# Performance work log

Measured on AMD Instinct MI355X. Metric: run time of the kernel, lower is better.

## Reference

```python
import jax, jax.numpy as jnp
import numpy as np

N = 100000      # nodes
E = 1600000     # edges (avg degree 16)
F_IN = 32       # node_features
F_OUT = 32      # filters
K = 2           # Chebyshev order


def setup_inputs() -> dict:
    key = jax.random.key(0)
    ks = jax.random.split(key, 8)
    x = jax.random.normal(ks[0], (N, F_IN), dtype=jnp.float32)
    edge_index = jax.random.randint(ks[1], (2, E), 0, N, dtype=jnp.int32).astype(jnp.int64)
    edge_weight = jax.random.uniform(ks[2], (E,), dtype=jnp.float32)
    s_in = 1.0 / np.sqrt(F_IN)
    s_out = 1.0 / np.sqrt(F_OUT)
    # gate order: i, f, c, o
    Wx = jax.random.normal(ks[3], (4, K, F_IN, F_OUT), dtype=jnp.float32) * s_in
    bx = jnp.zeros((4, F_OUT), dtype=jnp.float32)
    Wh = jax.random.normal(ks[4], (4, K, F_OUT, F_OUT), dtype=jnp.float32) * s_out
    bh = jnp.zeros((4, F_OUT), dtype=jnp.float32)
    wc = jax.random.normal(ks[5], (3, F_OUT), dtype=jnp.float32) * 0.1  # peephole i, f, o
    b_gate = jnp.zeros((4, F_OUT), dtype=jnp.float32)
    lin_w = jax.random.normal(ks[6], (F_OUT, 1), dtype=jnp.float32) * s_out
    lin_b = jnp.zeros((1,), dtype=jnp.float32)
    return dict(x=x, edge_index=edge_index, edge_weight=edge_weight, Wx=Wx, bx=bx,
                Wh=Wh, bh=bh, wc=wc, b_gate=b_gate, lin_w=lin_w, lin_b=lin_b)


def _cheb_norm(src, dst, w, num_nodes):
    # ChebConv 'sym' normalization with lambda_max = 2.0:
    # scaled Laplacian L_hat = L_sym - I has zero diagonal; off-diagonal entries are
    # -D^{-1/2} A D^{-1/2}. Self loops removed (equivalently: weight zeroed).
    w = jnp.where(src == dst, 0.0, w)
    deg = jax.ops.segment_sum(w, src, num_segments=num_nodes)
    dinv = jnp.where(deg > 0, jax.lax.rsqrt(jnp.where(deg > 0, deg, 1.0)), 0.0)
    return -dinv[src] * w * dinv[dst]


def _forward(x, src, dst, norm, Wx, bx, Wh, bh, wc, b_gate, lin_w, lin_b):
    n = x.shape[0]

    def cheb(inp, W, b):
        # K=2 Chebyshev conv: Tx_0 = inp, Tx_1 = L_hat @ inp (sparse gather/scatter)
        tx1 = jax.ops.segment_sum(norm[:, None] * inp[src], dst, num_segments=n)
        return inp @ W[0] + tx1 @ W[1] + b

    H = jnp.zeros((n, Wh.shape[-1]), dtype=x.dtype)
    C = jnp.zeros_like(H)
    I = jax.nn.sigmoid(cheb(x, Wx[0], bx[0]) + cheb(H, Wh[0], bh[0]) + wc[0] * C + b_gate[0])
    Fg = jax.nn.sigmoid(cheb(x, Wx[1], bx[1]) + cheb(H, Wh[1], bh[1]) + wc[1] * C + b_gate[1])
    T = jnp.tanh(cheb(x, Wx[2], bx[2]) + cheb(H, Wh[2], bh[2]) + b_gate[2])
    C = Fg * C + I * T
    O = jax.nn.sigmoid(cheb(x, Wx[3], bx[3]) + cheb(H, Wh[3], bh[3]) + wc[2] * C + b_gate[3])
    H = O * jnp.tanh(C)
    return jax.nn.relu(H) @ lin_w + lin_b  # [N, 1]


def reference(x, edge_index, edge_weight, Wx, bx, Wh, bh, wc, b_gate, lin_w, lin_b):
    src, dst = edge_index[0], edge_index[1]
    norm = _cheb_norm(src, dst, edge_weight, x.shape[0])
    return _forward(x, src, dst, norm, Wx, bx, Wh, bh, wc, b_gate, lin_w, lin_b)
```

## Files before the change

kernel.cpp:

```cpp
#include <hip/hip_runtime.h>


#define FDIM 32
#define MAX_N 100000
#define MAX_E 1600000
#define CBSH 8
#define CB 256
#define MAX_NB ((MAX_N + CB - 1) / CB)
#define NBLK 512
#define SCAN_TILE 2048
#define GNB 64
#define PERBLK 3136

typedef int   iv4 __attribute__((ext_vector_type(4)));
typedef float fv4 __attribute__((ext_vector_type(4)));
__device__ __forceinline__ iv4 nt_i4(const int* p)   { return __builtin_nontemporal_load((const iv4*)p); }
__device__ __forceinline__ fv4 nt_f4(const float* p) { return __builtin_nontemporal_load((const fv4*)p); }

__device__ float g_deg[MAX_N];
__device__ int   g_part2[2 * MAX_NB * NBLK + 1];
__device__ int   g_blk[1024];
__device__ uint2 g_rec[MAX_E];
__device__ uint2 g_srec[MAX_E];
__device__ int   g_row[MAX_N + 1];
__device__ __attribute__((aligned(16))) int   g_src2[MAX_E];
__device__ __attribute__((aligned(16))) float g_nrm2[MAX_E];
__device__ __attribute__((aligned(16))) float g_xs2[MAX_N * FDIM];
__device__ float g_tx1[MAX_N * FDIM];

__global__ __launch_bounds__(256) void hist2_kernel(const int* __restrict__ ei,
                                                    int E, int n_nodes, int nbuck,
                                                    int per_blk) {
    __shared__ int hd[MAX_NB];
    __shared__ int hs[MAX_NB];
    for (int i = threadIdx.x; i < nbuck; i += 256) { hd[i] = 0; hs[i] = 0; }
    __syncthreads();
    int start = blockIdx.x * per_blk;
    int end = start + per_blk;
    if (end > E) end = E;
    for (int base = start; base < end; base += 1024) {
        int e = base + threadIdx.x * 4;
        if (e + 4 <= end) {
            int4 s4 = *(const int4*)(ei + e);
            int4 d4 = *(const int4*)(ei + E + e);
#define H2(S, D) if ((unsigned)(S) < (unsigned)n_nodes && (unsigned)(D) < (unsigned)n_nodes) { \
                atomicAdd(&hd[(D) >> CBSH], 1); atomicAdd(&hs[(S) >> CBSH], 1); }
            H2(s4.x, d4.x) H2(s4.y, d4.y) H2(s4.z, d4.z) H2(s4.w, d4.w)
#undef H2
        } else if (e < end) {
            for (int q = e; q < end; ++q) {
                int s = ei[q], d = ei[E + q];
                if ((unsigned)s >= (unsigned)n_nodes || (unsigned)d >= (unsigned)n_nodes)
                    continue;
                atomicAdd(&hd[d >> CBSH], 1);
                atomicAdd(&hs[s >> CBSH], 1);
            }
        }
    }
    __syncthreads();
    for (int i = threadIdx.x; i < nbuck; i += 256) {
        g_part2[i * NBLK + blockIdx.x] = hd[i];
        g_part2[(nbuck + i) * NBLK + blockIdx.x] = hs[i];
    }
    if (blockIdx.x == 0 && threadIdx.x == 0)
        g_part2[2 * nbuck * NBLK] = 0;
}

__global__ __launch_bounds__(256) void scan1_kernel(int n) {
    __shared__ int sh[256];
    int tid = threadIdx.x;
    int base = blockIdx.x * SCAN_TILE + tid * 8;
    int v[8];
#pragma unroll
    for (int i = 0; i < 8; ++i) v[i] = (base + i < n) ? g_part2[base + i] : 0;
    int tsum = 0;
#pragma unroll
    for (int i = 0; i < 8; ++i) tsum += v[i];
    sh[tid] = tsum;
    __syncthreads();
    for (int off = 1; off < 256; off <<= 1) {
        int t = (tid >= off) ? sh[tid - off] : 0;
        __syncthreads();
        sh[tid] += t;
        __syncthreads();
    }
    if (tid == 255) g_blk[blockIdx.x] = sh[255];
    int run = sh[tid] - tsum;
#pragma unroll
    for (int i = 0; i < 8; ++i) {
        if (base + i < n) g_part2[base + i] = run;
        run += v[i];
    }
}

__global__ __launch_bounds__(256) void scatter_burst_kernel(const int* __restrict__ ei,
                                                            const float* __restrict__ w,
                                                            int E, int n_nodes, int nbuck,
                                                            int per_blk, int ntile) {
    __shared__ int   toff[256];
    __shared__ int   cnt[512];
    __shared__ int   sc[512];
    __shared__ int   gb[MAX_NB];
    __shared__ int   cur[MAX_NB];
    __shared__ uint2 staged[PERBLK];
    __shared__ int   gpos[PERBLK];
    int tid = threadIdx.x;
    int blk = blockIdx.x;
    int start = blk * per_blk;
    int end = start + per_blk;
    if (end > E) end = E;

    int orig = (tid < ntile) ? g_blk[tid] : 0;
    toff[tid] = orig;
    __syncthreads();
    for (int off = 1; off < 256; off <<= 1) {
        int v = (tid >= off) ? toff[tid - off] : 0;
        __syncthreads();
        toff[tid] += v;
        __syncthreads();
    }
    toff[tid] -= orig;
    __syncthreads();
#define SCN(idx) (g_part2[idx] + toff[(idx) >> 11])

    for (int phase = 0; phase < 2; ++phase) {
        cnt[tid] = 0; cnt[tid + 256] = 0;
        __syncthreads();
        for (int i = tid; i < nbuck; i += 256) {
            int flat = (phase * nbuck + i) * NBLK + blk;
            int g0 = SCN(flat);
            int g1 = SCN(flat + 1);
            gb[i] = g0 - phase * E;
            cnt[i] = g1 - g0;
        }
        __syncthreads();
        sc[tid] = cnt[tid]; sc[tid + 256] = cnt[tid + 256];
        __syncthreads();
        for (int off = 1; off < 512; off <<= 1) {
            int v0 = (tid >= off) ? sc[tid - off] : 0;
            int v1 = sc[tid + 256 - off];
            __syncthreads();
            sc[tid] += v0; sc[tid + 256] += v1;
            __syncthreads();
        }
        for (int i = tid; i < nbuck; i += 256) cur[i] = sc[i] - cnt[i];
        __syncthreads();
#define SB1(S, D, W)                                                            \
        {   int s = (S), d = (D);                                               \
            if ((unsigned)s < (unsigned)n_nodes && (unsigned)d < (unsigned)n_nodes) { \
                int key = phase ? s : d;                                        \
                int bin = key >> CBSH;                                          \
                float w0 = (s == d) ? 0.f : (W);           \
                unsigned pay = phase ? (unsigned)(s & (CB - 1))                 \
                    : (((unsigned)s << CBSH) | (unsigned)(d & (CB - 1)));       \
                int p = atomicAdd(&cur[bin], 1);                \
                staged[p] = make_uint2(pay, __float_as_uint(w0));               \
                gpos[p] = gb[bin] + (p - (sc[bin] - cnt[bin]));                 \
            } }
        for (int base = start; base < end; base += 1024) {
            int e = base + tid * 4;
            if (e + 4 <= end) {
                iv4 s4 = nt_i4(ei + e);
                iv4 d4 = nt_i4(ei + E + e);
                fv4 w4 = nt_f4(w + e);
                SB1(s4[0], d4[0], w4[0]) SB1(s4[1], d4[1], w4[1])
                SB1(s4[2], d4[2], w4[2]) SB1(s4[3], d4[3], w4[3])
            } else if (e < end) {
                for (int q = e; q < end; ++q) SB1(ei[q], ei[E + q], w[q])
            }
        }
#undef SB1
        __syncthreads();
        int tot = sc[511];
        if (phase == 0) {
            for (int t = tid; t < tot; t += 256) g_rec[gpos[t]] = staged[t];
        } else {
            for (int t = tid; t < tot; t += 256) g_srec[gpos[t]] = staged[t];
        }
        __syncthreads();
    }
#undef SCN
}

__global__ __launch_bounds__(1024) void sortdeg_kernel(const float* __restrict__ x,
                                                       int E, int n_nodes, int nbuck,
                                                       int ntile) {
    __shared__ int   toff[256];
    __shared__ int   cnt[CB];
    __shared__ int   cur[CB];
    __shared__ float ldeg[CB];
    __shared__ int   wsum[4];
    int tid = threadIdx.x;
    int b = blockIdx.x;

    int orig = 0;
    if (tid < 256) { orig = (tid < ntile) ? g_blk[tid] : 0; toff[tid] = orig; }
    __syncthreads();
    for (int off = 1; off < 256; off <<= 1) {
        int v = (tid < 256 && tid >= off) ? toff[tid - off] : 0;
        __syncthreads();
        if (tid < 256) toff[tid] += v;
        __syncthreads();
    }
    if (tid < 256) toff[tid] -= orig;
    if (tid < CB) { cnt[tid] = 0; ldeg[tid] = 0.f; }
    __syncthreads();
#define SCN(idx) (g_part2[idx] + toff[(idx) >> 11])
    int rsD = SCN(b * NBLK);
    int reD = SCN((b + 1) * NBLK);
    int rsS = SCN((nbuck + b) * NBLK) - E;
    int reS = SCN((nbuck + b + 1) * NBLK) - E;
#undef SCN

    for (int i = rsD + tid; i < reD; i += 1024)
        atomicAdd(&cnt[g_rec[i].x & (CB - 1)], 1);
    for (int i = rsS + tid; i < reS; i += 1024) {
        uint2 r = g_srec[i];
        atomicAdd(&ldeg[r.x], __uint_as_float(r.y));
    }
    __syncthreads();

    if (tid < CB) {
        float dg = ldeg[tid];
        float dv = (dg > 0.f) ? rsqrtf(dg) : 0.f;
        ldeg[tid] = dv;
        int node = (b << CBSH) + tid;
        if (node < n_nodes) g_deg[node] = dv;
    }
    __syncthreads();
    for (int t = tid; t < CB * FDIM / 4; t += 1024) {
        int q = t * 4;
        int loc = q >> 5;
        int node = (b << CBSH) + loc;
        if (node < n_nodes) {
            fv4 xv = *(const fv4*)&x[node * FDIM + (q & 31)];
            float dv = ldeg[loc];
            xv[0] *= dv; xv[1] *= dv; xv[2] *= dv; xv[3] *= dv;
            *(fv4*)&g_xs2[node * FDIM + (q & 31)] = xv;
        }
    }

    {
        int lane = tid & 63;
        int wave = tid >> 6;
        int v = (tid < CB) ? cnt[tid] : 0;
        int inc = v;
#pragma unroll
        for (int off = 1; off < 64; off <<= 1) {
            int t = __shfl_up(inc, off, 64);
            if (lane >= off) inc += t;
        }
        if (tid < CB && lane == 63) wsum[wave] = inc;
        __syncthreads();
        if (tid < CB) {
            int wo = 0;
#pragma unroll
            for (int ww = 0; ww < 4; ++ww) wo += (ww < wave) ? wsum[ww] : 0;
            int start = rsD + wo + (inc - v);
            cur[tid] = start;
            int node = (b << CBSH) + tid;
            if (node < n_nodes) g_row[node] = start;
        }
    }
    if (b == nbuck - 1 && tid == 0) g_row[n_nodes] = reD;
    __syncthreads();
    for (int i = rsD + tid; i < reD; i += 1024) {
        uint2 r = g_rec[i];
        int loc = r.x & (CB - 1);
        int pos = atomicAdd(&cur[loc], 1);
        g_src2[pos] = (int)(r.x >> CBSH);
        g_nrm2[pos] = -__uint_as_float(r.y);
    }
}

__global__ __launch_bounds__(256) void gather_kernel(int n_nodes) {
    int t = blockIdx.x * blockDim.x + threadIdx.x;
    int node = t >> 5;
    int f = t & 31;
    if (node >= n_nodes) return;
    int i = g_row[node];
    int end = g_row[node + 1];
    float acc = 0.f, accB = 0.f;
    while (i < end && (i & 3)) {
        acc += g_nrm2[i] * g_xs2[g_src2[i] * FDIM + f];
        ++i;
    }
    for (; i + 8 <= end; i += 8) {
        iv4 sa = nt_i4(g_src2 + i);
        iv4 sb = nt_i4(g_src2 + i + 4);
        fv4 na = nt_f4(g_nrm2 + i);
        fv4 nb = nt_f4(g_nrm2 + i + 4);
        float xa0 = g_xs2[sa[0] * FDIM + f], xa1 = g_xs2[sa[1] * FDIM + f];
        float xa2 = g_xs2[sa[2] * FDIM + f], xa3 = g_xs2[sa[3] * FDIM + f];
        float xb0 = g_xs2[sb[0] * FDIM + f], xb1 = g_xs2[sb[1] * FDIM + f];
        float xb2 = g_xs2[sb[2] * FDIM + f], xb3 = g_xs2[sb[3] * FDIM + f];
        acc  += na[0] * xa0 + na[1] * xa1 + na[2] * xa2 + na[3] * xa3;
        accB += nb[0] * xb0 + nb[1] * xb1 + nb[2] * xb2 + nb[3] * xb3;
    }
    for (; i + 4 <= end; i += 4) {
        iv4 s4 = nt_i4(g_src2 + i);
        fv4 n4 = nt_f4(g_nrm2 + i);
        acc += n4[0] * g_xs2[s4[0] * FDIM + f] + n4[1] * g_xs2[s4[1] * FDIM + f]
             + n4[2] * g_xs2[s4[2] * FDIM + f] + n4[3] * g_xs2[s4[3] * FDIM + f];
    }
    for (; i < end; ++i) acc += g_nrm2[i] * g_xs2[g_src2[i] * FDIM + f];
    float dvn = g_deg[node];
    g_tx1[node * FDIM + f] = dvn * (acc + accB);
}

__global__ __launch_bounds__(256, 4) void gates64_kernel(
    const float* __restrict__ x,
    const float* __restrict__ Wx, const float* __restrict__ bx,
    const float* __restrict__ bh, const float* __restrict__ wc,
    const float* __restrict__ bg, const float* __restrict__ lin_w,
    const float* __restrict__ lin_b, float* __restrict__ out, int n_nodes) {
    __shared__ float Ws[3 * 2048];
    __shared__ float xs[GNB * FDIM];
    __shared__ float ts[GNB * FDIM];

    for (int idx = threadIdx.x; idx < 512; idx += 256) {
        *(float4*)&Ws[idx * 4]        = *(const float4*)&Wx[0 * 2048 + idx * 4];
        *(float4*)&Ws[2048 + idx * 4] = *(const float4*)&Wx[2 * 2048 + idx * 4];
        *(float4*)&Ws[4096 + idx * 4] = *(const float4*)&Wx[3 * 2048 + idx * 4];
    }
    int node0 = blockIdx.x * GNB;
    for (int t = threadIdx.x; t < GNB * FDIM / 4; t += 256) {
        int q = t * 4;
        int n = node0 + (q >> 5);
        float4 xv = make_float4(0.f, 0.f, 0.f, 0.f);
        float4 tv = make_float4(0.f, 0.f, 0.f, 0.f);
        if (n < n_nodes) {
            xv = *(const float4*)&x[n * FDIM + (q & 31)];
            tv = *(const float4*)&g_tx1[n * FDIM + (q & 31)];
        }
        *(float4*)&xs[q] = xv;
        *(float4*)&ts[q] = tv;
    }
    __syncthreads();

    int j   = threadIdx.x & 31;
    int grp = threadIdx.x >> 5;

    float ai0=0.f,ai1=0.f,ai2=0.f,ai3=0.f,ai4=0.f,ai5=0.f,ai6=0.f,ai7=0.f;
    float ac0=0.f,ac1=0.f,ac2=0.f,ac3=0.f,ac4=0.f,ac5=0.f,ac6=0.f,ac7=0.f;
    float ao0=0.f,ao1=0.f,ao2=0.f,ao3=0.f,ao4=0.f,ao5=0.f,ao6=0.f,ao7=0.f;
    const float* xr = &xs[(grp * 8) * FDIM];
    const float* tr = &ts[(grp * 8) * FDIM];
    for (int k4 = 0; k4 < 32; k4 += 4) {
        float4 xv0 = *(const float4*)(xr + 0 * FDIM + k4);
        float4 xv1 = *(const float4*)(xr + 1 * FDIM + k4);
        float4 xv2 = *(const float4*)(xr + 2 * FDIM + k4);
        float4 xv3 = *(const float4*)(xr + 3 * FDIM + k4);
        float4 xv4 = *(const float4*)(xr + 4 * FDIM + k4);
        float4 xv5 = *(const float4*)(xr + 5 * FDIM + k4);
        float4 xv6 = *(const float4*)(xr + 6 * FDIM + k4);
        float4 xv7 = *(const float4*)(xr + 7 * FDIM + k4);
        float4 tv0 = *(const float4*)(tr + 0 * FDIM + k4);
        float4 tv1 = *(const float4*)(tr + 1 * FDIM + k4);
        float4 tv2 = *(const float4*)(tr + 2 * FDIM + k4);
        float4 tv3 = *(const float4*)(tr + 3 * FDIM + k4);
        float4 tv4 = *(const float4*)(tr + 4 * FDIM + k4);
        float4 tv5 = *(const float4*)(tr + 5 * FDIM + k4);
        float4 tv6 = *(const float4*)(tr + 6 * FDIM + k4);
        float4 tv7 = *(const float4*)(tr + 7 * FDIM + k4);
#define KSTEP(kc, COMP)                                        \
        {   int o0 = (k4 + kc) * 32 + j;                       \
            float wi0 = Ws[o0],        wi1 = Ws[1024 + o0];    \
            float wg0 = Ws[2048 + o0], wg1 = Ws[3072 + o0];    \
            float wo0 = Ws[4096 + o0], wo1 = Ws[5120 + o0];    \
            ai0 += xv0.COMP * wi0 + tv0.COMP * wi1;            \
            ac0 += xv0.COMP * wg0 + tv0.COMP * wg1;            \
            ao0 += xv0.COMP * wo0 + tv0.COMP * wo1;            \
            ai1 += xv1.COMP * wi0 + tv1.COMP * wi1;            \
            ac1 += xv1.COMP * wg0 + tv1.COMP * wg1;            \
            ao1 += xv1.COMP * wo0 + tv1.COMP * wo1;            \
            ai2 += xv2.COMP * wi0 + tv2.COMP * wi1;            \
            ac2 += xv2.COMP * wg0 + tv2.COMP * wg1;            \
            ao2 += xv2.COMP * wo0 + tv2.COMP * wo1;            \
            ai3 += xv3.COMP * wi0 + tv3.COMP * wi1;            \
            ac3 += xv3.COMP * wg0 + tv3.COMP * wg1;            \
            ao3 += xv3.COMP * wo0 + tv3.COMP * wo1;            \
            ai4 += xv4.COMP * wi0 + tv4.COMP * wi1;            \
            ac4 += xv4.COMP * wg0 + tv4.COMP * wg1;            \
            ao4 += xv4.COMP * wo0 + tv4.COMP * wo1;            \
            ai5 += xv5.COMP * wi0 + tv5.COMP * wi1;            \
            ac5 += xv5.COMP * wg0 + tv5.COMP * wg1;            \
            ao5 += xv5.COMP * wo0 + tv5.COMP * wo1;            \
            ai6 += xv6.COMP * wi0 + tv6.COMP * wi1;            \
            ac6 += xv6.COMP * wg0 + tv6.COMP * wg1;            \
            ao6 += xv6.COMP * wo0 + tv6.COMP * wo1;            \
            ai7 += xv7.COMP * wi0 + tv7.COMP * wi1;            \
            ac7 += xv7.COMP * wg0 + tv7.COMP * wg1;            \
            ao7 += xv7.COMP * wo0 + tv7.COMP * wo1;            \
        }
        KSTEP(0, x) KSTEP(1, y) KSTEP(2, z) KSTEP(3, w)
#undef KSTEP
    }

    float bi = bx[0 * 32 + j] + bh[0 * 32 + j] + bg[0 * 32 + j];
    float bc = bx[2 * 32 + j] + bh[2 * 32 + j] + bg[2 * 32 + j];
    float bo = bx[3 * 32 + j] + bh[3 * 32 + j] + bg[3 * 32 + j];
    float wcp = wc[2 * 32 + j];
    float lwj = lin_w[j];
    float lb0 = lin_b[0];

#define GOUT(m, AI, AC, AO)                                            \
    {   int n = node0 + grp * 8 + m;                                   \
        float I = 1.f / (1.f + __expf(-(AI + bi)));                    \
        float T = tanhf(AC + bc);                                      \
        float C = I * T;                                               \
        float O = 1.f / (1.f + __expf(-(AO + bo + wcp * C)));          \
        float H = O * tanhf(C);                                        \
        float r = fmaxf(H, 0.f) * lwj;                                 \
        _Pragma("unroll")                                              \
        for (int mm = 16; mm > 0; mm >>= 1) r += __shfl_xor(r, mm, 32);\
        if (j == 0 && n < n_nodes) out[n] = r + lb0; }
    GOUT(0, ai0, ac0, ao0) GOUT(1, ai1, ac1, ao1)
    GOUT(2, ai2, ac2, ao2) GOUT(3, ai3, ac3, ao3)
    GOUT(4, ai4, ac4, ao4) GOUT(5, ai5, ac5, ao5)
    GOUT(6, ai6, ac6, ao6) GOUT(7, ai7, ac7, ao7)
#undef GOUT
}

extern "C" void kernel_launch(void* const* d_in, const int* in_sizes, int n_in,
                              void* d_out, int out_size, void* d_ws, size_t ws_size,
                              hipStream_t stream) {
    const float* x     = (const float*)d_in[0];
    const int*   ei    = (const int*)d_in[1];
    const float* w     = (const float*)d_in[2];
    const float* Wx    = (const float*)d_in[3];
    const float* bx    = (const float*)d_in[4];
    const float* bh    = (const float*)d_in[6];
    const float* wc    = (const float*)d_in[7];
    const float* bg    = (const float*)d_in[8];
    const float* lin_w = (const float*)d_in[9];
    const float* lin_b = (const float*)d_in[10];
    float*       out   = (float*)d_out;

    int n_nodes = in_sizes[0] / FDIM;
    if (n_nodes > MAX_N) n_nodes = MAX_N;
    int E = in_sizes[2];
    if (E > MAX_E) E = MAX_E;

    int nbuck   = (n_nodes + CB - 1) >> CBSH;
    int per_blk = (((E + NBLK - 1) / NBLK) + 3) & ~3;
    int n_scan  = 2 * nbuck * NBLK + 1;
    int nb_scan = (n_scan + SCAN_TILE - 1) / SCAN_TILE;

    hist2_kernel<<<NBLK, 256, 0, stream>>>(ei, E, n_nodes, nbuck, per_blk);
    scan1_kernel<<<nb_scan, 256, 0, stream>>>(n_scan);
    scatter_burst_kernel<<<NBLK, 256, 0, stream>>>(ei, w, E, n_nodes, nbuck,
                                                   per_blk, nb_scan);
    sortdeg_kernel<<<nbuck, 1024, 0, stream>>>(x, E, n_nodes, nbuck, nb_scan);
    {
        long long tot = (long long)n_nodes * 32;
        gather_kernel<<<(int)((tot + 255) / 256), 256, 0, stream>>>(n_nodes);
    }
    gates64_kernel<<<(n_nodes + GNB - 1) / GNB, 256, 0, stream>>>(
        x, Wx, bx, bh, wc, bg, lin_w, lin_b, out, n_nodes);
}
```

Baseline: 254.7 us.

## Fold full symmetric normalization into edge weights and gather raw x

Splits the sort/degree kernel into a degree-sum kernel and a fine-sort kernel, so that all degrees exist before edges are placed. Each edge then stores its complete norm (-dinv[src]*w*dinv[dst]). This removes the pre-scaled copy of x (a full N×32 write plus read) and the per-node scale in the gather, which now reads x directly. In exchange it adds a kernel launch, a second pass over the scan offsets, and one random g_deg read per edge during the sort.

```diff
diff --git a/kernel.cpp b/kernel.cpp
--- a/kernel.cpp
+++ b/kernel.cpp
@@ -25,7 +25,6 @@
 __device__ int   g_row[MAX_N + 1];
 __device__ __attribute__((aligned(16))) int   g_src2[MAX_E];
 __device__ __attribute__((aligned(16))) float g_nrm2[MAX_E];
-__device__ __attribute__((aligned(16))) float g_xs2[MAX_N * FDIM];
 __device__ float g_tx1[MAX_N * FDIM];
 
 __global__ __launch_bounds__(256) void hist2_kernel(const int* __restrict__ ei,
@@ -182,17 +181,51 @@
 #undef SCN
 }
 
-__global__ __launch_bounds__(1024) void sortdeg_kernel(const float* __restrict__ x,
-                                                       int E, int n_nodes, int nbuck,
+__global__ __launch_bounds__(1024) void deg_sum_kernel(int E, int n_nodes, int nbuck,
                                                        int ntile) {
+    __shared__ int   toff[256];
+    __shared__ float ldeg[CB];
+    int tid = threadIdx.x;
+    int b = blockIdx.x;
+    int orig = 0;
+    if (tid < 256) { orig = (tid < ntile) ? g_blk[tid] : 0; toff[tid] = orig; }
+    __syncthreads();
+    for (int off = 1; off < 256; off <<= 1) {
+        int v = (tid < 256 && tid >= off) ? toff[tid - off] : 0;
+        __syncthreads();
+        if (tid < 256) toff[tid] += v;
+        __syncthreads();
+    }
+    if (tid < 256) toff[tid] -= orig;
+    if (tid < CB) ldeg[tid] = 0.f;
+    __syncthreads();
+#define SCN(idx) (g_part2[idx] + toff[(idx) >> 11])
+    int rs = SCN((nbuck + b) * NBLK) - E;
+    int re = SCN((nbuck + b + 1) * NBLK) - E;
+#undef SCN
+    for (int i = rs + tid; i < re; i += 1024) {
+        uint2 r = g_srec[i];
+        atomicAdd(&ldeg[r.x], __uint_as_float(r.y));
+    }
+    __syncthreads();
+    if (tid < CB) {
+        int node = (b << CBSH) + tid;
+        if (node < n_nodes) {
+            float dg = ldeg[tid];
+            g_deg[node] = (dg > 0.f) ? rsqrtf(dg) : 0.f;
+        }
+    }
+}
+
+__global__ __launch_bounds__(1024) void fine_sort_kernel(int E, int n_nodes, int nbuck,
+                                                         int ntile) {
     __shared__ int   toff[256];
     __shared__ int   cnt[CB];
     __shared__ int   cur[CB];
-    __shared__ float ldeg[CB];
+    __shared__ float dv[CB];
     __shared__ int   wsum[4];
     int tid = threadIdx.x;
     int b = blockIdx.x;
-
     int orig = 0;
     if (tid < 256) { orig = (tid < ntile) ? g_blk[tid] : 0; toff[tid] = orig; }
     __syncthreads();
@@ -203,43 +236,19 @@
         __syncthreads();
     }
     if (tid < 256) toff[tid] -= orig;
-    if (tid < CB) { cnt[tid] = 0; ldeg[tid] = 0.f; }
+    if (tid < CB) {
+        cnt[tid] = 0;
+        int node = (b << CBSH) + tid;
+        dv[tid] = (node < n_nodes) ? g_deg[node] : 0.f;
+    }
     __syncthreads();
 #define SCN(idx) (g_part2[idx] + toff[(idx) >> 11])
-    int rsD = SCN(b * NBLK);
-    int reD = SCN((b + 1) * NBLK);
-    int rsS = SCN((nbuck + b) * NBLK) - E;
-    int reS = SCN((nbuck + b + 1) * NBLK) - E;
+    int rs = SCN(b * NBLK);
+    int re = SCN((b + 1) * NBLK);
 #undef SCN
-
-    for (int i = rsD + tid; i < reD; i += 1024)
+    for (int i = rs + tid; i < re; i += 1024)
         atomicAdd(&cnt[g_rec[i].x & (CB - 1)], 1);
-    for (int i = rsS + tid; i < reS; i += 1024) {
-        uint2 r = g_srec[i];
-        atomicAdd(&ldeg[r.x], __uint_as_float(r.y));
-    }
-    __syncthreads();
-
-    if (tid < CB) {
-        float dg = ldeg[tid];
-        float dv = (dg > 0.f) ? rsqrtf(dg) : 0.f;
-        ldeg[tid] = dv;
-        int node = (b << CBSH) + tid;
-        if (node < n_nodes) g_deg[node] = dv;
-    }
-    __syncthreads();
-    for (int t = tid; t < CB * FDIM / 4; t += 1024) {
-        int q = t * 4;
-        int loc = q >> 5;
-        int node = (b << CBSH) + loc;
-        if (node < n_nodes) {
-            fv4 xv = *(const fv4*)&x[node * FDIM + (q & 31)];
-            float dv = ldeg[loc];
-            xv[0] *= dv; xv[1] *= dv; xv[2] *= dv; xv[3] *= dv;
-            *(fv4*)&g_xs2[node * FDIM + (q & 31)] = xv;
-        }
-    }
-
+    __syncthreads();
     {
         int lane = tid & 63;
         int wave = tid >> 6;
@@ -256,24 +265,27 @@
             int wo = 0;
 #pragma unroll
             for (int ww = 0; ww < 4; ++ww) wo += (ww < wave) ? wsum[ww] : 0;
-            int start = rsD + wo + (inc - v);
+            int start = rs + wo + (inc - v);
             cur[tid] = start;
             int node = (b << CBSH) + tid;
             if (node < n_nodes) g_row[node] = start;
         }
     }
-    if (b == nbuck - 1 && tid == 0) g_row[n_nodes] = reD;
-    __syncthreads();
-    for (int i = rsD + tid; i < reD; i += 1024) {
+    if (b == nbuck - 1 && tid == 0) g_row[n_nodes] = re;
+    __syncthreads();
+    for (int i = rs + tid; i < re; i += 1024) {
         uint2 r = g_rec[i];
+        int s = (int)(r.x >> CBSH);
         int loc = r.x & (CB - 1);
+        float nrm = -g_deg[s] * __uint_as_float(r.y) * dv[loc];
         int pos = atomicAdd(&cur[loc], 1);
-        g_src2[pos] = (int)(r.x >> CBSH);
-        g_nrm2[pos] = -__uint_as_float(r.y);
-    }
-}
-
-__global__ __launch_bounds__(256) void gather_kernel(int n_nodes) {
+        g_src2[pos] = s;
+        g_nrm2[pos] = nrm;
+    }
+}
+
+__global__ __launch_bounds__(256) void gather_kernel(const float* __restrict__ x,
+                                                     int n_nodes) {
     int t = blockIdx.x * blockDim.x + threadIdx.x;
     int node = t >> 5;
     int f = t & 31;
@@ -282,7 +294,7 @@
     int end = g_row[node + 1];
     float acc = 0.f, accB = 0.f;
     while (i < end && (i & 3)) {
-        acc += g_nrm2[i] * g_xs2[g_src2[i] * FDIM + f];
+        acc += g_nrm2[i] * x[g_src2[i] * FDIM + f];
         ++i;
     }
     for (; i + 8 <= end; i += 8) {
@@ -290,22 +302,21 @@
         iv4 sb = nt_i4(g_src2 + i + 4);
         fv4 na = nt_f4(g_nrm2 + i);
         fv4 nb = nt_f4(g_nrm2 + i + 4);
-        float xa0 = g_xs2[sa[0] * FDIM + f], xa1 = g_xs2[sa[1] * FDIM + f];
-        float xa2 = g_xs2[sa[2] * FDIM + f], xa3 = g_xs2[sa[3] * FDIM + f];
-        float xb0 = g_xs2[sb[0] * FDIM + f], xb1 = g_xs2[sb[1] * FDIM + f];
-        float xb2 = g_xs2[sb[2] * FDIM + f], xb3 = g_xs2[sb[3] * FDIM + f];
+        float xa0 = x[sa[0] * FDIM + f], xa1 = x[sa[1] * FDIM + f];
+        float xa2 = x[sa[2] * FDIM + f], xa3 = x[sa[3] * FDIM + f];
+        float xb0 = x[sb[0] * FDIM + f], xb1 = x[sb[1] * FDIM + f];
+        float xb2 = x[sb[2] * FDIM + f], xb3 = x[sb[3] * FDIM + f];
         acc  += na[0] * xa0 + na[1] * xa1 + na[2] * xa2 + na[3] * xa3;
         accB += nb[0] * xb0 + nb[1] * xb1 + nb[2] * xb2 + nb[3] * xb3;
     }
     for (; i + 4 <= end; i += 4) {
         iv4 s4 = nt_i4(g_src2 + i);
         fv4 n4 = nt_f4(g_nrm2 + i);
-        acc += n4[0] * g_xs2[s4[0] * FDIM + f] + n4[1] * g_xs2[s4[1] * FDIM + f]
-             + n4[2] * g_xs2[s4[2] * FDIM + f] + n4[3] * g_xs2[s4[3] * FDIM + f];
-    }
-    for (; i < end; ++i) acc += g_nrm2[i] * g_xs2[g_src2[i] * FDIM + f];
-    float dvn = g_deg[node];
-    g_tx1[node * FDIM + f] = dvn * (acc + accB);
+        acc += n4[0] * x[s4[0] * FDIM + f] + n4[1] * x[s4[1] * FDIM + f]
+             + n4[2] * x[s4[2] * FDIM + f] + n4[3] * x[s4[3] * FDIM + f];
+    }
+    for (; i < end; ++i) acc += g_nrm2[i] * x[g_src2[i] * FDIM + f];
+    g_tx1[node * FDIM + f] = acc + accB;
 }
 
 __global__ __launch_bounds__(256, 4) void gates64_kernel(
@@ -451,10 +462,11 @@
     scan1_kernel<<<nb_scan, 256, 0, stream>>>(n_scan);
     scatter_burst_kernel<<<NBLK, 256, 0, stream>>>(ei, w, E, n_nodes, nbuck,
                                                    per_blk, nb_scan);
-    sortdeg_kernel<<<nbuck, 1024, 0, stream>>>(x, E, n_nodes, nbuck, nb_scan);
+    deg_sum_kernel<<<nbuck, 1024, 0, stream>>>(E, n_nodes, nbuck, nb_scan);
+    fine_sort_kernel<<<nbuck, 1024, 0, stream>>>(E, n_nodes, nbuck, nb_scan);
     {
         long long tot = (long long)n_nodes * 32;
-        gather_kernel<<<(int)((tot + 255) / 256), 256, 0, stream>>>(n_nodes);
+        gather_kernel<<<(int)((tot + 255) / 256), 256, 0, stream>>>(x, n_nodes);
     }
     gates64_kernel<<<(n_nodes + GNB - 1) / GNB, 256, 0, stream>>>(
         x, Wx, bx, bh, wc, bg, lin_w, lin_b, out, n_nodes);
```

Measured after the change: 248.4 us. 1.03x faster.
